# Optimization experiments

Hardware: AMD Instinct MI355X
Metric: run time of the kernel (lower is better)

## Reference

```python
import jax, jax.numpy as jnp
import numpy as np
from jax import lax

WEIGHT_PREC = 8
ACT_PREC = 8
ACT_BOUND = 6.0  # fixed symmetric activation bound (quant_act.bounds)
EPS = 1e-6


def _ste_round(v):
    # AQT round-to-nearest with straight-through estimator
    return v + lax.stop_gradient(jnp.floor(v + 0.5) - v)


def setup_inputs() -> dict:
    key = jax.random.key(0)
    k1, k2 = jax.random.split(key)
    B, D, F = 131072, 512, 512
    x = jax.random.normal(k1, (B, D), dtype=jnp.float32)
    # lecun_normal-style kernel init
    kernel = jax.random.normal(k2, (D, F), dtype=jnp.float32) * (1.0 / np.sqrt(D))
    bias = jnp.zeros((F,), dtype=jnp.float32)
    padding_mask = jnp.ones((B, 1), dtype=bool)
    return {"x": x, "kernel": kernel, "bias": bias, "padding_mask": padding_mask}


def reference(x, kernel, bias, padding_mask):
    # padding_mask only affects bounds statistics collection; with fixed act
    # bounds and train=False it does not enter the math.
    wmax = float(2 ** (WEIGHT_PREC - 1) - 1)  # 127
    amax = float(2 ** (ACT_PREC - 1) - 1)     # 127

    # per-channel weight quantization: axis=(0,), scale shape (1, features)
    w_bound = jnp.maximum(jnp.max(jnp.abs(kernel), axis=0, keepdims=True), EPS)
    w_scale = wmax / w_bound                   # (1, F)
    w_q = jnp.clip(_ste_round(kernel * w_scale), -wmax, wmax)

    # per-tensor symmetric activation quantization with fixed bound
    a_scale = amax / ACT_BOUND                 # scalar
    x_q = jnp.clip(_ste_round(x * a_scale), -amax, amax)

    # integer-valued dot_general, then dequantize by the combined scale
    y = jnp.einsum('bd,df->bf', x_q, w_q)      # [B, F]
    y = y / (a_scale * w_scale)                # broadcast (1, F)
    return y + bias[jnp.newaxis, :]
```

## Files before the change

### kernel.cpp

```cpp
#include <hip/hip_runtime.h>
#include <stdint.h>

typedef int   int32x4   __attribute__((ext_vector_type(4)));
typedef int   int32x16  __attribute__((ext_vector_type(16)));
typedef float floatx4   __attribute__((ext_vector_type(4)));

#define B_ROWS 131072
#define DK 512
#define FN 512
#define A_SCALE_F ((float)(127.0 / 6.0))

#define GBLK 512
#define GT   512
#define BMS  32
#define GTILES (B_ROWS / BMS / GBLK)

__global__ void wq_quant_kernel(const float* __restrict__ kern,
                                int8_t* __restrict__ wq,
                                float* __restrict__ invcs) {
  __shared__ float smax[256];
  __shared__ float sscale[4];
  const int c = threadIdx.x & 3;
  const int g = threadIdx.x >> 2;
  const int col = blockIdx.x * 4 + c;

  float m = 0.f;
#pragma unroll
  for (int i = 0; i < 8; ++i) {
    m = fmaxf(m, fabsf(kern[(size_t)(g * 8 + i) * FN + col]));
  }
  smax[threadIdx.x] = m;
  __syncthreads();
  if (threadIdx.x < 4) {
    float mm = smax[threadIdx.x];
#pragma unroll 8
    for (int g2 = 1; g2 < 64; ++g2) mm = fmaxf(mm, smax[g2 * 4 + threadIdx.x]);
    const float wb = fmaxf(mm, 1e-6f);
    const float ws = 127.f / wb;
    sscale[threadIdx.x] = ws;
    invcs[blockIdx.x * 4 + threadIdx.x] =
        (float)(1.0 / ((double)A_SCALE_F * (double)ws));
  }
  __syncthreads();
  const float ws = sscale[c];
  uint32_t* wq32 = (uint32_t*)(wq + (size_t)col * DK);
#pragma unroll
  for (int d = 0; d < 2; ++d) {
    uint32_t p = 0;
#pragma unroll
    for (int j = 0; j < 4; ++j) {
      float v = kern[(size_t)(g * 8 + d * 4 + j) * FN + col] * ws;
      v = floorf(v + 0.5f);
      v = fminf(fmaxf(v, -127.f), 127.f);
      p |= ((uint32_t)((int)v & 255)) << (8 * j);
    }
    wq32[g * 2 + d] = p;
  }
}

__device__ __forceinline__ uint32_t quant4(floatx4 v) {
  uint32_t p = 0;
#pragma unroll
  for (int j = 0; j < 4; ++j) {
    float q = floorf(v[j] * A_SCALE_F + 0.5f);
    q = fminf(fmaxf(q, -127.f), 127.f);
    p |= ((uint32_t)((int)q & 255)) << (8 * j);
  }
  return p;
}

__global__ __launch_bounds__(GT, 2)
void aqt_gemm_fused(const float* __restrict__ x,
                    const int8_t* __restrict__ wq,
                    const float* __restrict__ invcs,
                    const float* __restrict__ bias,
                    float* __restrict__ out) {
  __shared__ __align__(16) uint8_t xq[2][BMS * DK];

  const int tid  = threadIdx.x;
  const int lane = tid & 63;
  const int wv   = tid >> 6;
  const int l31  = lane & 31;
  const int l5   = lane >> 5;

  const int c4 = tid & 127;
  const int rg = tid >> 7;

  const int col0 = wv * 64 + l31;
  const int col1 = col0 + 32;
  int32x4 Bf0[16], Bf1[16];
#pragma unroll
  for (int ks = 0; ks < 16; ++ks) {
    Bf0[ks] = *(const int32x4*)(wq + (size_t)col0 * DK + ks * 32 + l5 * 16);
    Bf1[ks] = *(const int32x4*)(wq + (size_t)col1 * DK + ks * 32 + l5 * 16);
  }
  const float inv0 = invcs[col0], bv0 = bias[col0];
  const float inv1 = invcs[col1], bv1 = bias[col1];

  const size_t row0 = (size_t)blockIdx.x * (GTILES * BMS);

#define LOADV(vdst, rt)                                                       \
  {                                                                           \
    const float* xg_ = x + (size_t)(rt) * DK;                                 \
    _Pragma("unroll")                                                         \
    for (int i_ = 0; i_ < 8; ++i_)                                            \
      vdst[i_] = *(const floatx4*)(xg_ + (size_t)(i_ * 4 + rg) * DK + c4 * 4);\
  }

#define QWRITE(vsrc, bufp)                                                    \
  {                                                                           \
    _Pragma("unroll")                                                         \
    for (int i_ = 0; i_ < 8; ++i_) {                                          \
      const int r_ = i_ * 4 + rg;                                             \
      *(uint32_t*)(&(bufp)[r_ * DK + ((c4 * 4) ^ ((r_ & 31) << 4))]) =        \
          quant4(vsrc[i_]);                                                   \
    }                                                                         \
  }

#define PANEL(Bf, colv, invv, bvv, bufp, rt)                                  \
  {                                                                           \
    int32x16 acc = (int32x16)(0);                                             \
    const uint8_t* aRow_ = (bufp) + l31 * DK;                                 \
    _Pragma("unroll")                                                         \
    for (int ks_ = 0; ks_ < 16; ++ks_) {                                      \
      int32x4 a_ = *(const int32x4*)(aRow_ + ((ks_ * 32 + l5 * 16) ^ (l31 << 4))); \
      acc = __builtin_amdgcn_mfma_i32_32x32x32_i8(a_, Bf[ks_], acc, 0, 0, 0); \
    }                                                                         \
    _Pragma("unroll")                                                         \
    for (int r_ = 0; r_ < 16; ++r_) {                                         \
      const int rowl_ = (r_ & 3) + 8 * (r_ >> 2) + 4 * l5;                    \
      __builtin_nontemporal_store((float)acc[r_] * (invv) + (bvv),            \
                                  &out[((rt) + rowl_) * FN + (colv)]);        \
    }                                                                         \
  }

  floatx4 vA[8], vB[8];

  LOADV(vA, row0);
  QWRITE(vA, (&xq[0][0]));
  LOADV(vB, row0 + BMS);
  asm volatile("s_waitcnt lgkmcnt(0)" ::: "memory");
  __builtin_amdgcn_s_barrier();

#pragma unroll 1
  for (int t = 0; t < GTILES; t += 2) {
    const size_t rowT = row0 + (size_t)t * BMS;

    if (t + 2 < GTILES) LOADV(vA, rowT + 2 * BMS);
    PANEL(Bf0, col0, inv0, bv0, (&xq[0][0]), rowT);
    PANEL(Bf1, col1, inv1, bv1, (&xq[0][0]), rowT);
    QWRITE(vB, (&xq[1][0]));
    asm volatile("s_waitcnt lgkmcnt(0)" ::: "memory");
    __builtin_amdgcn_s_barrier();

    if (t + 3 < GTILES) LOADV(vB, rowT + 3 * BMS);
    PANEL(Bf0, col0, inv0, bv0, (&xq[1][0]), rowT + BMS);
    PANEL(Bf1, col1, inv1, bv1, (&xq[1][0]), rowT + BMS);
    if (t + 2 < GTILES) QWRITE(vA, (&xq[0][0]));
    asm volatile("s_waitcnt lgkmcnt(0)" ::: "memory");
    __builtin_amdgcn_s_barrier();
  }

#undef LOADV
#undef QWRITE
#undef PANEL
}

extern "C" void kernel_launch(void* const* d_in, const int* in_sizes, int n_in,
                              void* d_out, int out_size, void* d_ws, size_t ws_size,
                              hipStream_t stream) {
  const float* x    = (const float*)d_in[0];
  const float* kern = (const float*)d_in[1];
  const float* bias = (const float*)d_in[2];

  int8_t* wq    = (int8_t*)d_ws;
  float*  invcs = (float*)((char*)d_ws + (size_t)FN * DK);

  wq_quant_kernel<<<128, 256, 0, stream>>>(kern, wq, invcs);
  aqt_gemm_fused<<<GBLK, GT, 0, stream>>>(x, wq, invcs, bias, (float*)d_out);
}
```

Before: 111.2 us.

## Stream weight fragments from cache instead of registers to raise occupancy

Weight fragments are no longer kept resident in registers. Each k-step now reloads them from global memory (L1/L2 cached), the loop becomes single-step double buffering with one register prefetch array, and the two output panels are interleaved in one MFMA loop. Launch bounds go from 2 to 4 blocks per CU to trade register pressure for more resident waves, so there is more latency hiding on this memory-bound kernel. The cost is extra global/cache load traffic per tile, plus less prefetch distance for x.

Result: slower. 250.8 us (+125.5%).

```diff
diff --git a/kernel.cpp b/kernel.cpp
--- a/kernel.cpp
+++ b/kernel.cpp
@@ -69,7 +69,7 @@
   return p;
 }
 
-__global__ __launch_bounds__(GT, 2)
+__global__ __launch_bounds__(GT, 4)
 void aqt_gemm_fused(const float* __restrict__ x,
                     const int8_t* __restrict__ wq,
                     const float* __restrict__ invcs,
@@ -88,12 +88,8 @@
 
   const int col0 = wv * 64 + l31;
   const int col1 = col0 + 32;
-  int32x4 Bf0[16], Bf1[16];
-#pragma unroll
-  for (int ks = 0; ks < 16; ++ks) {
-    Bf0[ks] = *(const int32x4*)(wq + (size_t)col0 * DK + ks * 32 + l5 * 16);
-    Bf1[ks] = *(const int32x4*)(wq + (size_t)col1 * DK + ks * 32 + l5 * 16);
-  }
+  const int8_t* bp0 = wq + (size_t)col0 * DK + l5 * 16;
+  const int8_t* bp1 = bp0 + (size_t)32 * DK;
   const float inv0 = invcs[col0], bv0 = bias[col0];
   const float inv1 = invcs[col1], bv1 = bias[col1];
 
@@ -117,53 +113,58 @@
     }                                                                         \
   }
 
-#define PANEL(Bf, colv, invv, bvv, bufp, rt)                                  \
-  {                                                                           \
-    int32x16 acc = (int32x16)(0);                                             \
-    const uint8_t* aRow_ = (bufp) + l31 * DK;                                 \
-    _Pragma("unroll")                                                         \
-    for (int ks_ = 0; ks_ < 16; ++ks_) {                                      \
-      int32x4 a_ = *(const int32x4*)(aRow_ + ((ks_ * 32 + l5 * 16) ^ (l31 << 4))); \
-      acc = __builtin_amdgcn_mfma_i32_32x32x32_i8(a_, Bf[ks_], acc, 0, 0, 0); \
-    }                                                                         \
-    _Pragma("unroll")                                                         \
-    for (int r_ = 0; r_ < 16; ++r_) {                                         \
-      const int rowl_ = (r_ & 3) + 8 * (r_ >> 2) + 4 * l5;                    \
-      __builtin_nontemporal_store((float)acc[r_] * (invv) + (bvv),            \
-                                  &out[((rt) + rowl_) * FN + (colv)]);        \
-    }                                                                         \
-  }
-
-  floatx4 vA[8], vB[8];
+  floatx4 vA[8];
 
   LOADV(vA, row0);
   QWRITE(vA, (&xq[0][0]));
-  LOADV(vB, row0 + BMS);
   asm volatile("s_waitcnt lgkmcnt(0)" ::: "memory");
   __builtin_amdgcn_s_barrier();
 
 #pragma unroll 1
-  for (int t = 0; t < GTILES; t += 2) {
+  for (int t = 0; t < GTILES; ++t) {
     const size_t rowT = row0 + (size_t)t * BMS;
+    const uint8_t* bufC = &xq[t & 1][0];
+    uint8_t* bufN = &xq[(t & 1) ^ 1][0];
+    const bool pf = (t + 1 < GTILES);
 
-    if (t + 2 < GTILES) LOADV(vA, rowT + 2 * BMS);
-    PANEL(Bf0, col0, inv0, bv0, (&xq[0][0]), rowT);
-    PANEL(Bf1, col1, inv1, bv1, (&xq[0][0]), rowT);
-    QWRITE(vB, (&xq[1][0]));
-    asm volatile("s_waitcnt lgkmcnt(0)" ::: "memory");
-    __builtin_amdgcn_s_barrier();
+    if (pf) LOADV(vA, rowT + BMS);
 
-    if (t + 3 < GTILES) LOADV(vB, rowT + 3 * BMS);
-    PANEL(Bf0, col0, inv0, bv0, (&xq[1][0]), rowT + BMS);
-    PANEL(Bf1, col1, inv1, bv1, (&xq[1][0]), rowT + BMS);
-    if (t + 2 < GTILES) QWRITE(vA, (&xq[0][0]));
+    int32x16 acc0 = (int32x16)(0);
+    int32x16 acc1 = (int32x16)(0);
+    {
+      const uint8_t* aRow = bufC + l31 * DK;
+      const int aswz = l31 << 4;
+#pragma unroll
+      for (int ks = 0; ks < 16; ++ks) {
+        int32x4 a  = *(const int32x4*)(aRow + ((ks * 32 + l5 * 16) ^ aswz));
+        int32x4 b0 = *(const int32x4*)(bp0 + ks * 32);
+        int32x4 b1 = *(const int32x4*)(bp1 + ks * 32);
+        acc0 = __builtin_amdgcn_mfma_i32_32x32x32_i8(a, b0, acc0, 0, 0, 0);
+        acc1 = __builtin_amdgcn_mfma_i32_32x32x32_i8(a, b1, acc1, 0, 0, 0);
+      }
+    }
+
+    if (pf) QWRITE(vA, bufN);
+
+#pragma unroll
+    for (int r = 0; r < 16; ++r) {
+      const int rowl = (r & 3) + 8 * (r >> 2) + 4 * l5;
+      __builtin_nontemporal_store((float)acc0[r] * inv0 + bv0,
+                                  &out[(rowT + rowl) * FN + col0]);
+    }
+#pragma unroll
+    for (int r = 0; r < 16; ++r) {
+      const int rowl = (r & 3) + 8 * (r >> 2) + 4 * l5;
+      __builtin_nontemporal_store((float)acc1[r] * inv1 + bv1,
+                                  &out[(rowT + rowl) * FN + col1]);
+    }
+
     asm volatile("s_waitcnt lgkmcnt(0)" ::: "memory");
     __builtin_amdgcn_s_barrier();
   }
 
 #undef LOADV
 #undef QWRITE
-#undef PANEL
 }
 
 extern "C" void kernel_launch(void* const* d_in, const int* in_sizes, int n_in,
```
